# Performance work log

Hardware: AMD Instinct MI355X
Metric: run time of the kernel (lower is better)

## Reference

```python
import jax, jax.numpy as jnp
import numpy as np

SWIGLU_LIMIT = 7.0
ALPHA = 1.702

def swiglu(x):
    # interleaved gate/linear halves, clamped, as in the torch module
    x_glu = x[..., ::2]
    x_lin = x[..., 1::2]
    x_glu = jnp.minimum(x_glu, SWIGLU_LIMIT)
    x_lin = jnp.clip(x_lin, -SWIGLU_LIMIT, SWIGLU_LIMIT)
    return x_glu * jax.nn.sigmoid(ALPHA * x_glu) * (x_lin + 1.0)

def setup_inputs() -> dict:
    key = jax.random.key(0)
    ks = jax.random.split(key, 6)
    B, K, E, H, I = 1024, 4, 16, 2048, 2048
    t = jax.random.normal(ks[0], (B, H), dtype=jnp.float32)
    expert_indices = jax.random.randint(ks[1], (B, K), 0, E, dtype=jnp.int32)
    gate_up_proj = jax.random.normal(ks[2], (E, 2 * I, H), dtype=jnp.float32) * 0.02
    gate_up_proj_bias = jax.random.normal(ks[3], (E, 2 * I), dtype=jnp.float32) * 0.02
    down_proj = jax.random.normal(ks[4], (E, H, I), dtype=jnp.float32) * 0.02
    down_proj_bias = jax.random.normal(ks[5], (E, H), dtype=jnp.float32) * 0.02
    return {"t": t, "expert_indices": expert_indices,
            "gate_up_proj": gate_up_proj, "gate_up_proj_bias": gate_up_proj_bias,
            "down_proj": down_proj, "down_proj_bias": down_proj_bias}

def reference(t, expert_indices, gate_up_proj, gate_up_proj_bias, down_proj, down_proj_bias):
    # Math-equivalent to the torch per-token weight gather: compute every token
    # against every expert, then gather the top_k selected expert outputs.
    # This avoids materializing the [B, K, 2I, H] gathered weight tensor.
    h = jnp.einsum('eck,bk->bec', gate_up_proj, t) + gate_up_proj_bias[None]  # [B,E,2I]
    h = swiglu(h)                                                              # [B,E,I]
    o = jnp.einsum('eck,bek->bec', down_proj, h) + down_proj_bias[None]        # [B,E,H]
    out = jnp.take_along_axis(o, expert_indices[:, :, None].astype(jnp.int32), axis=1)  # [B,K,H]
    return out
```

## Files before the change

kernel.cpp:

```cpp
#include <hip/hip_runtime.h>

typedef unsigned int uint32;
typedef __attribute__((ext_vector_type(8))) short short8;
typedef __attribute__((ext_vector_type(4))) float floatx4;

#define B_TOK 1024
#define TOPK 4
#define NEXP 16
#define H_DIM 2048
#define I_DIM 2048
#define NSLOT 4096
#define CAP 512
#define C1 4096
#define SLOT_ROWS 8192

#define TM 128
#define TN 128
#define BK 32
#define NTH 256

__device__ __forceinline__ unsigned short f2bf(float x) {
  unsigned int u = __float_as_uint(x);
  u += 0x7fffu + ((u >> 16) & 1u);
  return (unsigned short)(u >> 16);
}

__global__ void k_setup(const float* __restrict__ t, unsigned short* __restrict__ t_bf,
                        int* __restrict__ sorted_slots, int* __restrict__ counts) {
  int gid = blockIdx.x * blockDim.x + threadIdx.x;
  const float4* tp = (const float4*)t;
  float4 v = tp[gid];
  ushort4 o;
  o.x = f2bf(v.x); o.y = f2bf(v.y); o.z = f2bf(v.z); o.w = f2bf(v.w);
  ((ushort4*)t_bf)[gid] = o;
  if (gid < SLOT_ROWS) sorted_slots[gid] = 0;
  if (gid < NEXP) counts[gid] = 0;
}

__global__ void k_scatter(const int* __restrict__ eidx,
                          int* __restrict__ sorted_slots, int* __restrict__ counts) {
  int slot = blockIdx.x * blockDim.x + threadIdx.x;
  if (slot >= NSLOT) return;
  int e = eidx[slot];
  int j = atomicAdd(counts + e, 1);
  if (j < CAP) sorted_slots[e * CAP + j] = slot;
}

__global__ __launch_bounds__(NTH) void k_gemm1(
    const unsigned short* __restrict__ t_bf, const float* __restrict__ Wg,
    const float* __restrict__ bg, const int* __restrict__ sorted_slots,
    const int* __restrict__ counts, unsigned short* __restrict__ h_act) {
  const int e = blockIdx.y >> 2;
  const int m0 = (blockIdx.y & 3) * TM;
  int cnt = counts[e]; cnt = cnt > CAP ? CAP : cnt;
  if (m0 >= cnt) return;
  const int mr = min(cnt - m0, TM);
  const int c0 = blockIdx.x * TN;
  const int base = e * CAP + m0;

  __shared__ unsigned short smA[TM * BK];
  __shared__ unsigned short smB[TN * BK];

  const int tid = threadIdx.x;
  const int kq = tid & 3;
  const int r0 = tid >> 2;
  const int r1 = r0 + 64;

  const int tok0 = sorted_slots[base + r0] >> 2;
  const int tok1 = sorted_slots[base + r1] >> 2;
  const unsigned short* pA0 = t_bf + (size_t)tok0 * H_DIM + kq * 8;
  const unsigned short* pA1 = t_bf + (size_t)tok1 * H_DIM + kq * 8;
  const float* pB0 = Wg + ((size_t)e * C1 + (size_t)(c0 + r0)) * H_DIM + kq * 8;
  const float* pB1 = Wg + ((size_t)e * C1 + (size_t)(c0 + r1)) * H_DIM + kq * 8;

  unsigned short* wA0 = smA + r0 * BK + kq * 8;
  unsigned short* wA1 = smA + r1 * BK + kq * 8;
  unsigned short* wB0 = smB + r0 * BK + kq * 8;
  unsigned short* wB1 = smB + r1 * BK + kq * 8;

  const int wave = tid >> 6;
  const int lane = tid & 63;
  const int wm = wave & 1, wn = wave >> 1;
  const int l15 = lane & 15;
  const int k8 = (lane >> 4) * 8;
  const unsigned short* fa = smA + (wm * 64 + l15) * BK + k8;
  const unsigned short* fb = smB + (wn * 64 + l15) * BK + k8;

  floatx4 acc[4][4];
#pragma unroll
  for (int i = 0; i < 4; ++i)
#pragma unroll
    for (int j = 0; j < 4; ++j) acc[i][j] = (floatx4){0.f, 0.f, 0.f, 0.f};

  for (int k0 = 0; k0 < H_DIM; k0 += BK) {
    uint4 a0 = *(const uint4*)(pA0 + k0);
    uint4 a1 = *(const uint4*)(pA1 + k0);
    float4 b00 = *(const float4*)(pB0 + k0);
    float4 b01 = *(const float4*)(pB0 + k0 + 4);
    float4 b10 = *(const float4*)(pB1 + k0);
    float4 b11 = *(const float4*)(pB1 + k0 + 4);
    uint4 w0, w1;
    w0.x = (uint32)f2bf(b00.x) | ((uint32)f2bf(b00.y) << 16);
    w0.y = (uint32)f2bf(b00.z) | ((uint32)f2bf(b00.w) << 16);
    w0.z = (uint32)f2bf(b01.x) | ((uint32)f2bf(b01.y) << 16);
    w0.w = (uint32)f2bf(b01.z) | ((uint32)f2bf(b01.w) << 16);
    w1.x = (uint32)f2bf(b10.x) | ((uint32)f2bf(b10.y) << 16);
    w1.y = (uint32)f2bf(b10.z) | ((uint32)f2bf(b10.w) << 16);
    w1.z = (uint32)f2bf(b11.x) | ((uint32)f2bf(b11.y) << 16);
    w1.w = (uint32)f2bf(b11.z) | ((uint32)f2bf(b11.w) << 16);
    *(uint4*)wA0 = a0;
    *(uint4*)wA1 = a1;
    *(uint4*)wB0 = w0;
    *(uint4*)wB1 = w1;
    __syncthreads();
    short8 af[4], bfr[4];
#pragma unroll
    for (int i = 0; i < 4; ++i) af[i] = *(const short8*)(fa + i * 16 * BK);
#pragma unroll
    for (int j = 0; j < 4; ++j) bfr[j] = *(const short8*)(fb + j * 16 * BK);
#pragma unroll
    for (int i = 0; i < 4; ++i)
#pragma unroll
      for (int j = 0; j < 4; ++j)
        acc[i][j] = __builtin_amdgcn_mfma_f32_16x16x32_bf16(af[i], bfr[j], acc[i][j], 0, 0, 0);
    __syncthreads();
  }

  const int rq = (lane >> 4) * 4;
#pragma unroll
  for (int j = 0; j < 4; ++j) {
    const int c = c0 + wn * 64 + j * 16 + l15;
    const float bias = bg[e * C1 + c];
    const int ic = c >> 1;
#pragma unroll
    for (int i = 0; i < 4; ++i) {
      const int rbase = wm * 64 + i * 16 + rq;
#pragma unroll
      for (int r = 0; r < 4; ++r) {
        float v = acc[i][j][r] + bias;
        float o = __shfl_xor(v, 1);
        if ((lane & 1) == 0) {
          float xg = fminf(v, 7.0f);
          float xl = fminf(fmaxf(o, -7.0f), 7.0f);
          float res = (xg / (1.0f + __expf(-1.702f * xg))) * (xl + 1.0f);
          const int rl = rbase + r;
          if (rl < mr) h_act[(size_t)(base + rl) * I_DIM + ic] = f2bf(res);
        }
      }
    }
  }
}

__global__ __launch_bounds__(NTH) void k_gemm2(
    const unsigned short* __restrict__ h_act, const float* __restrict__ Wd,
    const float* __restrict__ bd, const int* __restrict__ sorted_slots,
    const int* __restrict__ counts, float* __restrict__ out) {
  const int e = blockIdx.y >> 2;
  const int m0 = (blockIdx.y & 3) * TM;
  int cnt = counts[e]; cnt = cnt > CAP ? CAP : cnt;
  if (m0 >= cnt) return;
  const int mr = min(cnt - m0, TM);
  const int c0 = blockIdx.x * TN;
  const int base = e * CAP + m0;

  __shared__ unsigned short smA[TM * BK];
  __shared__ unsigned short smB[TN * BK];

  const int tid = threadIdx.x;
  const int kq = tid & 3;
  const int r0 = tid >> 2;
  const int r1 = r0 + 64;

  const unsigned short* pA0 = h_act + (size_t)(base + r0) * I_DIM + kq * 8;
  const unsigned short* pA1 = h_act + (size_t)(base + r1) * I_DIM + kq * 8;
  const float* pB0 = Wd + ((size_t)e * H_DIM + (size_t)(c0 + r0)) * I_DIM + kq * 8;
  const float* pB1 = Wd + ((size_t)e * H_DIM + (size_t)(c0 + r1)) * I_DIM + kq * 8;

  unsigned short* wA0 = smA + r0 * BK + kq * 8;
  unsigned short* wA1 = smA + r1 * BK + kq * 8;
  unsigned short* wB0 = smB + r0 * BK + kq * 8;
  unsigned short* wB1 = smB + r1 * BK + kq * 8;

  const int wave = tid >> 6;
  const int lane = tid & 63;
  const int wm = wave & 1, wn = wave >> 1;
  const int l15 = lane & 15;
  const int k8 = (lane >> 4) * 8;
  const unsigned short* fa = smA + (wm * 64 + l15) * BK + k8;
  const unsigned short* fb = smB + (wn * 64 + l15) * BK + k8;

  floatx4 acc[4][4];
#pragma unroll
  for (int i = 0; i < 4; ++i)
#pragma unroll
    for (int j = 0; j < 4; ++j) acc[i][j] = (floatx4){0.f, 0.f, 0.f, 0.f};

  for (int k0 = 0; k0 < I_DIM; k0 += BK) {
    uint4 a0 = *(const uint4*)(pA0 + k0);
    uint4 a1 = *(const uint4*)(pA1 + k0);
    float4 b00 = *(const float4*)(pB0 + k0);
    float4 b01 = *(const float4*)(pB0 + k0 + 4);
    float4 b10 = *(const float4*)(pB1 + k0);
    float4 b11 = *(const float4*)(pB1 + k0 + 4);
    uint4 w0, w1;
    w0.x = (uint32)f2bf(b00.x) | ((uint32)f2bf(b00.y) << 16);
    w0.y = (uint32)f2bf(b00.z) | ((uint32)f2bf(b00.w) << 16);
    w0.z = (uint32)f2bf(b01.x) | ((uint32)f2bf(b01.y) << 16);
    w0.w = (uint32)f2bf(b01.z) | ((uint32)f2bf(b01.w) << 16);
    w1.x = (uint32)f2bf(b10.x) | ((uint32)f2bf(b10.y) << 16);
    w1.y = (uint32)f2bf(b10.z) | ((uint32)f2bf(b10.w) << 16);
    w1.z = (uint32)f2bf(b11.x) | ((uint32)f2bf(b11.y) << 16);
    w1.w = (uint32)f2bf(b11.z) | ((uint32)f2bf(b11.w) << 16);
    *(uint4*)wA0 = a0;
    *(uint4*)wA1 = a1;
    *(uint4*)wB0 = w0;
    *(uint4*)wB1 = w1;
    __syncthreads();
    short8 af[4], bfr[4];
#pragma unroll
    for (int i = 0; i < 4; ++i) af[i] = *(const short8*)(fa + i * 16 * BK);
#pragma unroll
    for (int j = 0; j < 4; ++j) bfr[j] = *(const short8*)(fb + j * 16 * BK);
#pragma unroll
    for (int i = 0; i < 4; ++i)
#pragma unroll
      for (int j = 0; j < 4; ++j)
        acc[i][j] = __builtin_amdgcn_mfma_f32_16x16x32_bf16(af[i], bfr[j], acc[i][j], 0, 0, 0);
    __syncthreads();
  }

  const int rq = (lane >> 4) * 4;
#pragma unroll
  for (int j = 0; j < 4; ++j) {
    const int c = c0 + wn * 64 + j * 16 + l15;
    const float bias = bd[e * H_DIM + c];
#pragma unroll
    for (int i = 0; i < 4; ++i) {
      const int rbase = wm * 64 + i * 16 + rq;
#pragma unroll
      for (int r = 0; r < 4; ++r) {
        const int rl = rbase + r;
        if (rl < mr) {
          const int slot = sorted_slots[base + rl];
          out[(size_t)slot * H_DIM + c] = acc[i][j][r] + bias;
        }
      }
    }
  }
}

extern "C" void kernel_launch(void* const* d_in, const int* in_sizes, int n_in,
                              void* d_out, int out_size, void* d_ws, size_t ws_size,
                              hipStream_t stream) {
  const float* t = (const float*)d_in[0];
  const int* eidx = (const int*)d_in[1];
  const float* Wg = (const float*)d_in[2];
  const float* bg = (const float*)d_in[3];
  const float* Wd = (const float*)d_in[4];
  const float* bd = (const float*)d_in[5];
  float* out = (float*)d_out;

  char* ws = (char*)d_ws;
  unsigned short* t_bf = (unsigned short*)ws;
  unsigned short* h_act = (unsigned short*)(ws + (size_t)4 * 1024 * 1024);
  int* sorted_slots = (int*)(ws + (size_t)36 * 1024 * 1024);
  int* counts = (int*)(ws + (size_t)36 * 1024 * 1024 + (size_t)SLOT_ROWS * 4);

  k_setup<<<dim3((B_TOK * H_DIM / 4) / 256), dim3(256), 0, stream>>>(t, t_bf, sorted_slots, counts);
  k_scatter<<<dim3(NSLOT / 256), dim3(256), 0, stream>>>(eidx, sorted_slots, counts);
  k_gemm1<<<dim3(C1 / TN, NEXP * (CAP / TM)), dim3(NTH), 0, stream>>>(t_bf, Wg, bg, sorted_slots, counts, h_act);
  k_gemm2<<<dim3(H_DIM / TN, NEXP * (CAP / TM)), dim3(NTH), 0, stream>>>(h_act, Wd, bd, sorted_slots, counts, out);
}
```

Measured before the change: 1.095 ms.

## Double-buffer LDS tiles with register prefetch, XOR swizzle, and faster bf16 packing

Both expert GEMM kernels now use two LDS buffers. The next K-tile's global loads are issued before the MFMA work on the current tile and written to the other buffer afterwards, so each step needs one barrier instead of two. LDS rows get an XOR swizzle on the 8-element chunk index to reduce bank conflicts on fragment reads. The fp32-to-bf16 weight conversion switches to a cheaper add-and-byte-permute packing, which rounds half away from zero instead of to nearest even. In exchange, LDS use doubles and more registers stay live, which may lower occupancy.

```diff
diff --git a/kernel.cpp b/kernel.cpp
--- a/kernel.cpp
+++ b/kernel.cpp
@@ -23,6 +23,12 @@
   unsigned int u = __float_as_uint(x);
   u += 0x7fffu + ((u >> 16) & 1u);
   return (unsigned short)(u >> 16);
+}
+
+__device__ __forceinline__ uint32 pk2bf(float a, float b) {
+  uint32 ua = __float_as_uint(a) + 0x8000u;
+  uint32 ub = __float_as_uint(b) + 0x8000u;
+  return __builtin_amdgcn_perm(ub, ua, 0x07060302u);
 }
 
 __global__ void k_setup(const float* __restrict__ t, unsigned short* __restrict__ t_bf,
@@ -58,13 +64,14 @@
   const int c0 = blockIdx.x * TN;
   const int base = e * CAP + m0;
 
-  __shared__ unsigned short smA[TM * BK];
-  __shared__ unsigned short smB[TN * BK];
+  __shared__ unsigned short smA[2][TM * BK];
+  __shared__ unsigned short smB[2][TN * BK];
 
   const int tid = threadIdx.x;
   const int kq = tid & 3;
   const int r0 = tid >> 2;
   const int r1 = r0 + 64;
+  const int sw = (r0 >> 1) & 3;
 
   const int tok0 = sorted_slots[base + r0] >> 2;
   const int tok1 = sorted_slots[base + r1] >> 2;
@@ -73,18 +80,17 @@
   const float* pB0 = Wg + ((size_t)e * C1 + (size_t)(c0 + r0)) * H_DIM + kq * 8;
   const float* pB1 = Wg + ((size_t)e * C1 + (size_t)(c0 + r1)) * H_DIM + kq * 8;
 
-  unsigned short* wA0 = smA + r0 * BK + kq * 8;
-  unsigned short* wA1 = smA + r1 * BK + kq * 8;
-  unsigned short* wB0 = smB + r0 * BK + kq * 8;
-  unsigned short* wB1 = smB + r1 * BK + kq * 8;
+  const int offA0 = r0 * BK + (kq ^ sw) * 8;
+  const int offA1 = r1 * BK + (kq ^ sw) * 8;
+  const int offB0 = offA0;
+  const int offB1 = offA1;
 
   const int wave = tid >> 6;
   const int lane = tid & 63;
   const int wm = wave & 1, wn = wave >> 1;
   const int l15 = lane & 15;
-  const int k8 = (lane >> 4) * 8;
-  const unsigned short* fa = smA + (wm * 64 + l15) * BK + k8;
-  const unsigned short* fb = smB + (wn * 64 + l15) * BK + k8;
+  const int kc = lane >> 4;
+  const int kcs = (kc ^ ((l15 >> 1) & 3)) * 8;
 
   floatx4 acc[4][4];
 #pragma unroll
@@ -92,38 +98,62 @@
 #pragma unroll
     for (int j = 0; j < 4; ++j) acc[i][j] = (floatx4){0.f, 0.f, 0.f, 0.f};
 
-  for (int k0 = 0; k0 < H_DIM; k0 += BK) {
-    uint4 a0 = *(const uint4*)(pA0 + k0);
-    uint4 a1 = *(const uint4*)(pA1 + k0);
-    float4 b00 = *(const float4*)(pB0 + k0);
-    float4 b01 = *(const float4*)(pB0 + k0 + 4);
-    float4 b10 = *(const float4*)(pB1 + k0);
-    float4 b11 = *(const float4*)(pB1 + k0 + 4);
+  uint4 a0 = *(const uint4*)(pA0);
+  uint4 a1 = *(const uint4*)(pA1);
+  float4 b00 = *(const float4*)(pB0);
+  float4 b01 = *(const float4*)(pB0 + 4);
+  float4 b10 = *(const float4*)(pB1);
+  float4 b11 = *(const float4*)(pB1 + 4);
+  {
+    *(uint4*)&smA[0][offA0] = a0;
+    *(uint4*)&smA[0][offA1] = a1;
     uint4 w0, w1;
-    w0.x = (uint32)f2bf(b00.x) | ((uint32)f2bf(b00.y) << 16);
-    w0.y = (uint32)f2bf(b00.z) | ((uint32)f2bf(b00.w) << 16);
-    w0.z = (uint32)f2bf(b01.x) | ((uint32)f2bf(b01.y) << 16);
-    w0.w = (uint32)f2bf(b01.z) | ((uint32)f2bf(b01.w) << 16);
-    w1.x = (uint32)f2bf(b10.x) | ((uint32)f2bf(b10.y) << 16);
-    w1.y = (uint32)f2bf(b10.z) | ((uint32)f2bf(b10.w) << 16);
-    w1.z = (uint32)f2bf(b11.x) | ((uint32)f2bf(b11.y) << 16);
-    w1.w = (uint32)f2bf(b11.z) | ((uint32)f2bf(b11.w) << 16);
-    *(uint4*)wA0 = a0;
-    *(uint4*)wA1 = a1;
-    *(uint4*)wB0 = w0;
-    *(uint4*)wB1 = w1;
+    w0.x = pk2bf(b00.x, b00.y); w0.y = pk2bf(b00.z, b00.w);
+    w0.z = pk2bf(b01.x, b01.y); w0.w = pk2bf(b01.z, b01.w);
+    w1.x = pk2bf(b10.x, b10.y); w1.y = pk2bf(b10.z, b10.w);
+    w1.z = pk2bf(b11.x, b11.y); w1.w = pk2bf(b11.z, b11.w);
+    *(uint4*)&smB[0][offB0] = w0;
+    *(uint4*)&smB[0][offB1] = w1;
+  }
+
+  const int nk = H_DIM / BK;
+#pragma unroll 2
+  for (int kk = 0; kk < nk; ++kk) {
     __syncthreads();
+    const int buf = kk & 1;
+    const bool more = (kk + 1) < nk;
+    if (more) {
+      const int ko = (kk + 1) * BK;
+      a0 = *(const uint4*)(pA0 + ko);
+      a1 = *(const uint4*)(pA1 + ko);
+      b00 = *(const float4*)(pB0 + ko);
+      b01 = *(const float4*)(pB0 + ko + 4);
+      b10 = *(const float4*)(pB1 + ko);
+      b11 = *(const float4*)(pB1 + ko + 4);
+    }
     short8 af[4], bfr[4];
 #pragma unroll
-    for (int i = 0; i < 4; ++i) af[i] = *(const short8*)(fa + i * 16 * BK);
-#pragma unroll
-    for (int j = 0; j < 4; ++j) bfr[j] = *(const short8*)(fb + j * 16 * BK);
+    for (int i = 0; i < 4; ++i)
+      af[i] = *(const short8*)&smA[buf][(wm * 64 + i * 16 + l15) * BK + kcs];
+#pragma unroll
+    for (int j = 0; j < 4; ++j)
+      bfr[j] = *(const short8*)&smB[buf][(wn * 64 + j * 16 + l15) * BK + kcs];
 #pragma unroll
     for (int i = 0; i < 4; ++i)
 #pragma unroll
       for (int j = 0; j < 4; ++j)
         acc[i][j] = __builtin_amdgcn_mfma_f32_16x16x32_bf16(af[i], bfr[j], acc[i][j], 0, 0, 0);
-    __syncthreads();
+    if (more) {
+      *(uint4*)&smA[buf ^ 1][offA0] = a0;
+      *(uint4*)&smA[buf ^ 1][offA1] = a1;
+      uint4 w0, w1;
+      w0.x = pk2bf(b00.x, b00.y); w0.y = pk2bf(b00.z, b00.w);
+      w0.z = pk2bf(b01.x, b01.y); w0.w = pk2bf(b01.z, b01.w);
+      w1.x = pk2bf(b10.x, b10.y); w1.y = pk2bf(b10.z, b10.w);
+      w1.z = pk2bf(b11.x, b11.y); w1.w = pk2bf(b11.z, b11.w);
+      *(uint4*)&smB[buf ^ 1][offB0] = w0;
+      *(uint4*)&smB[buf ^ 1][offB1] = w1;
+    }
   }
 
   const int rq = (lane >> 4) * 4;
@@ -163,31 +193,29 @@
   const int c0 = blockIdx.x * TN;
   const int base = e * CAP + m0;
 
-  __shared__ unsigned short smA[TM * BK];
-  __shared__ unsigned short smB[TN * BK];
+  __shared__ unsigned short smA[2][TM * BK];
+  __shared__ unsigned short smB[2][TN * BK];
 
   const int tid = threadIdx.x;
   const int kq = tid & 3;
   const int r0 = tid >> 2;
   const int r1 = r0 + 64;
+  const int sw = (r0 >> 1) & 3;
 
   const unsigned short* pA0 = h_act + (size_t)(base + r0) * I_DIM + kq * 8;
   const unsigned short* pA1 = h_act + (size_t)(base + r1) * I_DIM + kq * 8;
   const float* pB0 = Wd + ((size_t)e * H_DIM + (size_t)(c0 + r0)) * I_DIM + kq * 8;
   const float* pB1 = Wd + ((size_t)e * H_DIM + (size_t)(c0 + r1)) * I_DIM + kq * 8;
 
-  unsigned short* wA0 = smA + r0 * BK + kq * 8;
-  unsigned short* wA1 = smA + r1 * BK + kq * 8;
-  unsigned short* wB0 = smB + r0 * BK + kq * 8;
-  unsigned short* wB1 = smB + r1 * BK + kq * 8;
+  const int offA0 = r0 * BK + (kq ^ sw) * 8;
+  const int offA1 = r1 * BK + (kq ^ sw) * 8;
 
   const int wave = tid >> 6;
   const int lane = tid & 63;
   const int wm = wave & 1, wn = wave >> 1;
   const int l15 = lane & 15;
-  const int k8 = (lane >> 4) * 8;
-  const unsigned short* fa = smA + (wm * 64 + l15) * BK + k8;
-  const unsigned short* fb = smB + (wn * 64 + l15) * BK + k8;
+  const int kc = lane >> 4;
+  const int kcs = (kc ^ ((l15 >> 1) & 3)) * 8;
 
   floatx4 acc[4][4];
 #pragma unroll
@@ -195,38 +223,62 @@
 #pragma unroll
     for (int j = 0; j < 4; ++j) acc[i][j] = (floatx4){0.f, 0.f, 0.f, 0.f};
 
-  for (int k0 = 0; k0 < I_DIM; k0 += BK) {
-    uint4 a0 = *(const uint4*)(pA0 + k0);
-    uint4 a1 = *(const uint4*)(pA1 + k0);
-    float4 b00 = *(const float4*)(pB0 + k0);
-    float4 b01 = *(const float4*)(pB0 + k0 + 4);
-    float4 b10 = *(const float4*)(pB1 + k0);
-    float4 b11 = *(const float4*)(pB1 + k0 + 4);
+  uint4 a0 = *(const uint4*)(pA0);
+  uint4 a1 = *(const uint4*)(pA1);
+  float4 b00 = *(const float4*)(pB0);
+  float4 b01 = *(const float4*)(pB0 + 4);
+  float4 b10 = *(const float4*)(pB1);
+  float4 b11 = *(const float4*)(pB1 + 4);
+  {
+    *(uint4*)&smA[0][offA0] = a0;
+    *(uint4*)&smA[0][offA1] = a1;
     uint4 w0, w1;
-    w0.x = (uint32)f2bf(b00.x) | ((uint32)f2bf(b00.y) << 16);
-    w0.y = (uint32)f2bf(b00.z) | ((uint32)f2bf(b00.w) << 16);
-    w0.z = (uint32)f2bf(b01.x) | ((uint32)f2bf(b01.y) << 16);
-    w0.w = (uint32)f2bf(b01.z) | ((uint32)f2bf(b01.w) << 16);
-    w1.x = (uint32)f2bf(b10.x) | ((uint32)f2bf(b10.y) << 16);
-    w1.y = (uint32)f2bf(b10.z) | ((uint32)f2bf(b10.w) << 16);
-    w1.z = (uint32)f2bf(b11.x) | ((uint32)f2bf(b11.y) << 16);
-    w1.w = (uint32)f2bf(b11.z) | ((uint32)f2bf(b11.w) << 16);
-    *(uint4*)wA0 = a0;
-    *(uint4*)wA1 = a1;
-    *(uint4*)wB0 = w0;
-    *(uint4*)wB1 = w1;
+    w0.x = pk2bf(b00.x, b00.y); w0.y = pk2bf(b00.z, b00.w);
+    w0.z = pk2bf(b01.x, b01.y); w0.w = pk2bf(b01.z, b01.w);
+    w1.x = pk2bf(b10.x, b10.y); w1.y = pk2bf(b10.z, b10.w);
+    w1.z = pk2bf(b11.x, b11.y); w1.w = pk2bf(b11.z, b11.w);
+    *(uint4*)&smB[0][offA0] = w0;
+    *(uint4*)&smB[0][offA1] = w1;
+  }
+
+  const int nk = I_DIM / BK;
+#pragma unroll 2
+  for (int kk = 0; kk < nk; ++kk) {
     __syncthreads();
+    const int buf = kk & 1;
+    const bool more = (kk + 1) < nk;
+    if (more) {
+      const int ko = (kk + 1) * BK;
+      a0 = *(const uint4*)(pA0 + ko);
+      a1 = *(const uint4*)(pA1 + ko);
+      b00 = *(const float4*)(pB0 + ko);
+      b01 = *(const float4*)(pB0 + ko + 4);
+      b10 = *(const float4*)(pB1 + ko);
+      b11 = *(const float4*)(pB1 + ko + 4);
+    }
     short8 af[4], bfr[4];
 #pragma unroll
-    for (int i = 0; i < 4; ++i) af[i] = *(const short8*)(fa + i * 16 * BK);
-#pragma unroll
-    for (int j = 0; j < 4; ++j) bfr[j] = *(const short8*)(fb + j * 16 * BK);
+    for (int i = 0; i < 4; ++i)
+      af[i] = *(const short8*)&smA[buf][(wm * 64 + i * 16 + l15) * BK + kcs];
+#pragma unroll
+    for (int j = 0; j < 4; ++j)
+      bfr[j] = *(const short8*)&smB[buf][(wn * 64 + j * 16 + l15) * BK + kcs];
 #pragma unroll
     for (int i = 0; i < 4; ++i)
 #pragma unroll
       for (int j = 0; j < 4; ++j)
         acc[i][j] = __builtin_amdgcn_mfma_f32_16x16x32_bf16(af[i], bfr[j], acc[i][j], 0, 0, 0);
-    __syncthreads();
+    if (more) {
+      *(uint4*)&smA[buf ^ 1][offA0] = a0;
+      *(uint4*)&smA[buf ^ 1][offA1] = a1;
+      uint4 w0, w1;
+      w0.x = pk2bf(b00.x, b00.y); w0.y = pk2bf(b00.z, b00.w);
+      w0.z = pk2bf(b01.x, b01.y); w0.w = pk2bf(b01.z, b01.w);
+      w1.x = pk2bf(b10.x, b10.y); w1.y = pk2bf(b10.z, b10.w);
+      w1.z = pk2bf(b11.x, b11.y); w1.w = pk2bf(b11.z, b11.w);
+      *(uint4*)&smB[buf ^ 1][offA0] = w0;
+      *(uint4*)&smB[buf ^ 1][offA1] = w1;
+    }
   }
 
   const int rq = (lane >> 4) * 4;
```

After: 1.072 ms. -2.1%, faster.
